# Kernel optimization log

Measured on AMD Instinct MI355X. Metric: run time of the kernel, lower is better.

The kernel has to match this reference:

```python
import jax, jax.numpy as jnp
import numpy as np
from jax import lax

B, S, D = 2, 1024, 1024
N = 16            # mamba state dim
EXPAND = 2
DI = EXPAND * D   # inner dim 2048
K = 4             # depthwise conv kernel
H = 16            # soliton heads
DH = D // H
DT_RANK = D // 16
SOL_DT = 0.1      # soliton integration step


def _ln(x, g, b):
    mu = jnp.mean(x, -1, keepdims=True)
    var = jnp.var(x, -1, keepdims=True)
    return (x - mu) / jnp.sqrt(var + 1e-5) * g + b


def setup_inputs() -> dict:
    key = jax.random.key(0)
    ks = jax.random.split(key, 12)
    def nrm(k, sh, sc=0.02):
        return jax.random.normal(k, sh, jnp.float32) * sc
    return {
        'x': nrm(ks[0], (B, S, D), 1.0),
        'ln1_g': jnp.ones(D), 'ln1_b': jnp.zeros(D),
        'W_in': nrm(ks[1], (D, 2 * DI)), 'b_in': jnp.zeros(2 * DI),
        'conv_w': nrm(ks[2], (DI, K), 0.1), 'conv_b': jnp.zeros(DI),
        'W_xp': nrm(ks[3], (DI, DT_RANK + 2 * N)),
        'W_dt': nrm(ks[4], (DT_RANK, DI), 0.1),
        'b_dt': jnp.full((DI,), -4.6),  # softplus(-4.6) ~ 0.01 init dt
        'A_log': jnp.log(jnp.broadcast_to(jnp.arange(1, N + 1, dtype=jnp.float32), (DI, N))),
        'D_skip': jnp.ones(DI),
        'W_out': nrm(ks[5], (DI, D)), 'b_out': jnp.zeros(D),
        'ln2_g': jnp.ones(D), 'ln2_b': jnp.zeros(D),
        'W_si': nrm(ks[6], (D, D)), 'b_si': jnp.zeros(D),
        'gates': nrm(ks[7], (H, 3), 0.1),   # per-head weights for [sine-Gordon, KdV, Heimburg-Jackson]
        'alpha': nrm(ks[8], (H,), 0.1),     # HJ nonlinearity coefficient
        'W_so': nrm(ks[9], (D, D)), 'b_so': jnp.zeros(D),
    }


def _forward(x, ln1_g, ln1_b, W_in, b_in, conv_w, conv_b, W_xp, W_dt, b_dt,
             A_log, D_skip, W_out, b_out, ln2_g, ln2_b, W_si, b_si,
             gates, alpha, W_so, b_so):
    b, s, d = x.shape
    # ---- Mamba mixer branch ----
    u = _ln(x, ln1_g, ln1_b)
    xz = u @ W_in + b_in                                   # [b,s,2*DI]
    xp, z = jnp.split(xz, 2, axis=-1)                      # [b,s,DI] each
    # causal depthwise conv along sequence
    xt = xp.transpose(0, 2, 1)                             # [b,DI,s]
    yc = lax.conv_general_dilated(xt, conv_w[:, None, :], (1,), [(K - 1, 0)],
                                  feature_group_count=DI,
                                  dimension_numbers=('NCW', 'OIW', 'NCW'))
    xc = jax.nn.silu(yc.transpose(0, 2, 1) + conv_b)       # [b,s,DI]
    dbc = xc @ W_xp
    dtr, Bs, Cs = jnp.split(dbc, [DT_RANK, DT_RANK + N], axis=-1)
    dt = jax.nn.softplus(dtr @ W_dt + b_dt)                # [b,s,DI]
    A = -jnp.exp(A_log)                                    # [DI,N]
    dA = jnp.exp(dt[..., None] * A)                        # [b,s,DI,N]
    dBx = (dt * xc)[..., None] * Bs[:, :, None, :]         # [b,s,DI,N]

    def step(h, inp):
        dA_t, dBx_t, C_t = inp
        h = dA_t * h + dBx_t                               # [b,DI,N]
        y = jnp.einsum('bdn,bn->bd', h, C_t)
        return h, y

    h0 = jnp.zeros((b, DI, N), x.dtype)
    xs = (dA.transpose(1, 0, 2, 3), dBx.transpose(1, 0, 2, 3), Cs.transpose(1, 0, 2))
    _, ys = lax.scan(step, h0, xs)
    y = ys.transpose(1, 0, 2)                              # [b,s,DI]
    y = (y + xc * D_skip) * jax.nn.silu(z)
    x = x + y @ W_out + b_out

    # ---- Soliton interaction branch ----
    v = _ln(x, ln2_g, ln2_b)
    uu = (v @ W_si + b_si).reshape(b, s, H, DH)
    up = jnp.pad(uu, ((0, 0), (2, 2), (0, 0), (0, 0)), mode='edge')
    ux = (up[:, 3:-1] - up[:, 1:-3]) * 0.5                 # central 1st derivative
    uxx = up[:, 3:-1] - 2.0 * uu + up[:, 1:-3]
    uxxx = (up[:, 4:] - 2.0 * up[:, 3:-1] + 2.0 * up[:, 1:-3] - up[:, :-4]) * 0.5
    sg = jnp.sin(uu)                                       # sine-Gordon
    kdv = -6.0 * uu * ux - uxxx                            # KdV
    hj = (1.0 + alpha[None, None, :, None] * uu) * uxx     # Heimburg-Jackson
    du = (gates[None, None, :, 0:1] * sg
          + gates[None, None, :, 1:2] * kdv
          + gates[None, None, :, 2:3] * hj)
    sol = (SOL_DT * du).reshape(b, s, d) @ W_so + b_so
    return x + sol


def reference(x, ln1_g, ln1_b, W_in, b_in, conv_w, conv_b, W_xp, W_dt, b_dt,
              A_log, D_skip, W_out, b_out, ln2_g, ln2_b, W_si, b_si,
              gates, alpha, W_so, b_so):
    return _forward(x, ln1_g, ln1_b, W_in, b_in, conv_w, conv_b, W_xp, W_dt, b_dt,
                    A_log, D_skip, W_out, b_out, ln2_g, ln2_b, W_si, b_si,
                    gates, alpha, W_so, b_so)
```

## Files before the change

kernel.cpp:

```cpp
#include <hip/hip_runtime.h>
#include <hip/hip_bf16.h>
#include <math.h>

typedef unsigned short u16;
typedef unsigned int u32;
typedef __attribute__((ext_vector_type(8))) short short8;
typedef __attribute__((ext_vector_type(4))) float f32x4;

constexpr int CB = 2;
constexpr int CS = 1024;
constexpr int CD = 1024;
constexpr int CDI = 2048;
constexpr int CNC2 = 64;
constexpr int CL2 = 16;

__device__ inline u16 f2bf(float v) {
  __hip_bfloat16 h = __float2bfloat16(v);
  return *reinterpret_cast<u16*>(&h);
}
__device__ inline float bf2f(u16 v) {
  return __uint_as_float(((u32)v) << 16);
}

__device__ inline void gload16(const void* g, void* l) {
  __builtin_amdgcn_global_load_lds((const __attribute__((address_space(1))) void*)g,
                                   (__attribute__((address_space(3))) void*)l, 16, 0, 0);
}

struct TJob { const float* src; u16* dst; int K, N, gx, base; };
struct TJobs { TJob j[6]; };

__global__ __launch_bounds__(256)
void transpose_all_kernel(TJobs jobs) {
  int b = blockIdx.x;
  int ji = 0;
#pragma unroll
  for (int i = 1; i < 6; ++i) if (b >= jobs.j[i].base) ji = i;
  TJob jb = jobs.j[ji];
  int lb = b - jb.base;
  int n0 = (lb % jb.gx) * 32, k0 = (lb / jb.gx) * 32;
  __shared__ float tile[32][33];
  int tx = threadIdx.x & 31, ty = threadIdx.x >> 5;
#pragma unroll
  for (int i = 0; i < 4; ++i) {
    int k = k0 + ty + i * 8, n = n0 + tx;
    tile[ty + i * 8][tx] = (n < jb.N) ? jb.src[(size_t)k * jb.N + n] : 0.f;
  }
  __syncthreads();
#pragma unroll
  for (int i = 0; i < 4; ++i) {
    int n = n0 + ty + i * 8, k = k0 + tx;
    jb.dst[(size_t)n * jb.K + k] = f2bf(tile[tx][ty + i * 8]);
  }
}

__global__ __launch_bounds__(256)
void ln_kernel(const float* __restrict__ x, const float* __restrict__ g,
               const float* __restrict__ bb, u16* __restrict__ outb) {
  int row = blockIdx.x;
  const float4* xr = (const float4*)(x + (size_t)row * CD);
  float4 v = xr[threadIdx.x];
  float s = v.x + v.y + v.z + v.w;
  float ss = v.x * v.x + v.y * v.y + v.z * v.z + v.w * v.w;
#pragma unroll
  for (int o = 1; o < 64; o <<= 1) { s += __shfl_xor(s, o); ss += __shfl_xor(ss, o); }
  __shared__ float sb[4], ssb[4];
  int wid = threadIdx.x >> 6;
  if ((threadIdx.x & 63) == 0) { sb[wid] = s; ssb[wid] = ss; }
  __syncthreads();
  s = sb[0] + sb[1] + sb[2] + sb[3];
  ss = ssb[0] + ssb[1] + ssb[2] + ssb[3];
  float mu = s * (1.f / CD);
  float var = ss * (1.f / CD) - mu * mu;
  float rstd = rsqrtf(var + 1e-5f);
  float4 gv = ((const float4*)g)[threadIdx.x];
  float4 bv = ((const float4*)bb)[threadIdx.x];
  ushort4 o;
  o.x = f2bf((v.x - mu) * rstd * gv.x + bv.x);
  o.y = f2bf((v.y - mu) * rstd * gv.y + bv.y);
  o.z = f2bf((v.z - mu) * rstd * gv.z + bv.z);
  o.w = f2bf((v.w - mu) * rstd * gv.w + bv.w);
  ((ushort4*)(outb + (size_t)row * CD))[threadIdx.x] = o;
}

__global__ __launch_bounds__(256)
void ln_fuse_kernel(const float* __restrict__ x, const float* __restrict__ S0,
                    const float* __restrict__ S1, const float* __restrict__ bo,
                    const float* __restrict__ g, const float* __restrict__ bb,
                    float* __restrict__ out, u16* __restrict__ outb) {
  int row = blockIdx.x;
  float4 xv = ((const float4*)(x + (size_t)row * CD))[threadIdx.x];
  float4 s0 = ((const float4*)(S0 + (size_t)row * CD))[threadIdx.x];
  float4 s1 = ((const float4*)(S1 + (size_t)row * CD))[threadIdx.x];
  float4 bv0 = ((const float4*)bo)[threadIdx.x];
  float4 v;
  v.x = xv.x + s0.x + s1.x + bv0.x;
  v.y = xv.y + s0.y + s1.y + bv0.y;
  v.z = xv.z + s0.z + s1.z + bv0.z;
  v.w = xv.w + s0.w + s1.w + bv0.w;
  ((float4*)(out + (size_t)row * CD))[threadIdx.x] = v;
  float s = v.x + v.y + v.z + v.w;
  float ss = v.x * v.x + v.y * v.y + v.z * v.z + v.w * v.w;
#pragma unroll
  for (int o = 1; o < 64; o <<= 1) { s += __shfl_xor(s, o); ss += __shfl_xor(ss, o); }
  __shared__ float sb[4], ssb[4];
  int wid = threadIdx.x >> 6;
  if ((threadIdx.x & 63) == 0) { sb[wid] = s; ssb[wid] = ss; }
  __syncthreads();
  s = sb[0] + sb[1] + sb[2] + sb[3];
  ss = ssb[0] + ssb[1] + ssb[2] + ssb[3];
  float mu = s * (1.f / CD);
  float var = ss * (1.f / CD) - mu * mu;
  float rstd = rsqrtf(var + 1e-5f);
  float4 gv = ((const float4*)g)[threadIdx.x];
  float4 bv = ((const float4*)bb)[threadIdx.x];
  ushort4 o;
  o.x = f2bf((v.x - mu) * rstd * gv.x + bv.x);
  o.y = f2bf((v.y - mu) * rstd * gv.y + bv.y);
  o.z = f2bf((v.z - mu) * rstd * gv.z + bv.z);
  o.w = f2bf((v.w - mu) * rstd * gv.w + bv.w);
  ((ushort4*)(outb + (size_t)row * CD))[threadIdx.x] = o;
}

__global__ __launch_bounds__(256)
void add3_kernel(float* __restrict__ out, const float* __restrict__ S0,
                 const float* __restrict__ S1, const float* __restrict__ bias) {
  int idx = blockIdx.x * 256 + threadIdx.x;
  int c4 = idx & 255;
  float4 o = ((const float4*)out)[idx];
  float4 a = ((const float4*)S0)[idx];
  float4 b = ((const float4*)S1)[idx];
  float4 bv = ((const float4*)bias)[c4];
  o.x += a.x + b.x + bv.x;
  o.y += a.y + b.y + bv.y;
  o.z += a.z + b.z + bv.z;
  o.w += a.w + b.w + bv.w;
  ((float4*)out)[idx] = o;
}

template<int BN, int LDA, int LDB>
__global__ __launch_bounds__(256)
void gemm5_kernel(const u16* __restrict__ A, const u16* __restrict__ Bt,
                  const float* __restrict__ bias,
                  const float* __restrict__ resid, int ldr,
                  float* __restrict__ C, int ldc,
                  u16* __restrict__ aux, int auxN,
                  int partial_stride, int Nact, int K, int act) {
  constexpr int WN = BN / 32;
  constexpr int AHALF = 128 * 32;
  constexpr int BHALF = BN * 32;
  __shared__ __align__(16) u16 As[2 * AHALF];
  __shared__ __align__(16) u16 Bs[2 * BHALF];
  const int tid = threadIdx.x, lane = tid & 63, wid = tid >> 6;
  const int wr = wid >> 1, wc = wid & 1;
  int nwg = gridDim.x * gridDim.y;
  int bid = blockIdx.y * gridDim.x + blockIdx.x;
  int swz = (bid & 7) * (nwg >> 3) + (bid >> 3);
  int bx = swz % gridDim.x, by = swz / gridDim.x;
  const int bm = by * 128, bn = bx * BN;
  const int kper = K / gridDim.z;
  const int kbeg = blockIdx.z * kper;
  const int nt = kper / 32;

  int a_src[2], b_src[BN / 64];
#pragma unroll
  for (int j = 0; j < 2; ++j) {
    int c = tid + j * 256;
    int row = c >> 2, kc = (c & 3) ^ ((row + (row >> 2)) & 3);
    a_src[j] = (bm + row) * LDA + kc * 8 + kbeg;
  }
#pragma unroll
  for (int j = 0; j < BN / 64; ++j) {
    int c = tid + j * 256;
    int row = c >> 2, kc = (c & 3) ^ ((row + (row >> 2)) & 3);
    b_src[j] = (bn + row) * LDB + kc * 8 + kbeg;
  }
  int afo[4], bfo[WN];
  const int ch = lane >> 4;
#pragma unroll
  for (int m = 0; m < 4; ++m) {
    int r = wr * 64 + m * 16 + (lane & 15);
    afo[m] = r * 32 + ((ch ^ ((r + (r >> 2)) & 3)) << 3);
  }
#pragma unroll
  for (int n = 0; n < WN; ++n) {
    int r = wc * (BN / 2) + n * 16 + (lane & 15);
    bfo[n] = r * 32 + ((ch ^ ((r + (r >> 2)) & 3)) << 3);
  }
  f32x4 acc[4][WN] = {};

  auto stage = [&](int t, int abuf, int bbuf) {
    int k0 = t * 32;
#pragma unroll
    for (int j = 0; j < 2; ++j)
      gload16(A + a_src[j] + k0, As + abuf + (tid + j * 256) * 8);
#pragma unroll
    for (int j = 0; j < BN / 64; ++j)
      gload16(Bt + b_src[j] + k0, Bs + bbuf + (tid + j * 256) * 8);
  };
  auto compute = [&](int abuf, int bbuf) {
    short8 af[4], bfr[WN];
#pragma unroll
    for (int m = 0; m < 4; ++m) af[m] = *(const short8*)&As[abuf + afo[m]];
#pragma unroll
    for (int n = 0; n < WN; ++n) bfr[n] = *(const short8*)&Bs[bbuf + bfo[n]];
#pragma unroll
    for (int m = 0; m < 4; ++m)
#pragma unroll
      for (int n = 0; n < WN; ++n)
        acc[m][n] = __builtin_amdgcn_mfma_f32_16x16x32_bf16(af[m], bfr[n], acc[m][n], 0, 0, 0);
  };

  stage(0, 0, 0);
  __syncthreads();
  int t = 0;
  while (true) {
    if (t + 1 < nt) stage(t + 1, AHALF, BHALF);
    compute(0, 0);
    __syncthreads();
    if (++t == nt) break;
    if (t + 1 < nt) stage(t + 1, 0, 0);
    compute(AHALF, BHALF);
    __syncthreads();
    if (++t == nt) break;
  }

  const int fr = lane & 15, fq = lane >> 4;
  const int ksegs = gridDim.z;
  float* Cz = C + (size_t)blockIdx.z * partial_stride;
#pragma unroll
  for (int m = 0; m < 4; ++m) {
#pragma unroll
    for (int n = 0; n < WN; ++n) {
#pragma unroll
      for (int j = 0; j < 4; ++j) {
        int row = bm + wr * 64 + m * 16 + fq * 4 + j;
        int col = bn + wc * (BN / 2) + n * 16 + fr;
        if (col < Nact) {
          float v = acc[m][n][j];
          if (ksegs == 1) {
            if (bias) v += bias[col];
            if (resid) v += resid[(size_t)row * ldr + col];
            if (act == 1) v = (v > 20.f) ? v : log1pf(__expf(v));
            if (C) C[(size_t)row * ldc + col] = v;
            if (aux && col < auxN) aux[(size_t)row * auxN + col] = f2bf(v);
          } else if (partial_stride > 0) {
            Cz[(size_t)row * ldc + col] = v;
          } else {
            atomicAdd(&C[(size_t)row * ldc + col], v);
          }
        }
      }
    }
  }
}

__global__ __launch_bounds__(256)
void conv_silu_kernel(const u16* __restrict__ xz, const float* __restrict__ w,
                      const float* __restrict__ cb, u16* __restrict__ xcb) {
  int idx = blockIdx.x * 256 + threadIdx.x;
  int d0 = (idx & 255) * 8;
  int t = (idx >> 8) & (CS - 1);
  int b = idx >> 18;
  const u16* base = xz + (size_t)(b * CS) * 4096 + d0;
  float acc[8];
  float4 cb2[2] = { ((const float4*)(cb + d0))[0], ((const float4*)(cb + d0))[1] };
#pragma unroll
  for (int i = 0; i < 8; ++i) acc[i] = ((const float*)cb2)[i];
#pragma unroll
  for (int k = 0; k < 4; ++k) {
    int tt = t - 3 + k;
    if (tt >= 0) {
      short8 v = *(const short8*)(base + (size_t)tt * 4096);
#pragma unroll
      for (int i = 0; i < 8; ++i)
        acc[i] = fmaf(bf2f((u16)v[i]), w[(d0 + i) * 4 + k], acc[i]);
    }
  }
  short8 o;
#pragma unroll
  for (int i = 0; i < 8; ++i) {
    float v = acc[i] * (1.f / (1.f + __expf(-acc[i])));
    o[i] = (short)f2bf(v);
  }
  *(short8*)(xcb + (size_t)(b * CS + t) * CDI + d0) = o;
}

__global__ __launch_bounds__(256)
void dtr_convert_kernel(const float* __restrict__ dbc, u16* __restrict__ dtrb) {
  int idx = blockIdx.x * 256 + threadIdx.x;
  int r = idx >> 6, k = idx & 63;
  dtrb[idx] = f2bf(dbc[r * 96 + k]);
}

__global__ __launch_bounds__(256)
void scan1_kernel(const u16* __restrict__ dtb, const u16* __restrict__ xcb,
                  const float* __restrict__ dbc, const float* __restrict__ A_log,
                  u16* __restrict__ P, u16* __restrict__ Q) {
  int gid = blockIdx.x * 256 + threadIdx.x;
  int d = gid & (CDI - 1);
  int c = (gid >> 11) & (CNC2 - 1);
  int b = gid >> 17;
  float acoef[16];
#pragma unroll
  for (int j = 0; j < 4; ++j) {
    float4 al = ((const float4*)(A_log + d * 16))[j];
    acoef[j * 4 + 0] = -__expf(al.x);
    acoef[j * 4 + 1] = -__expf(al.y);
    acoef[j * 4 + 2] = -__expf(al.z);
    acoef[j * 4 + 3] = -__expf(al.w);
  }
  float Pv[16], Qv[16];
#pragma unroll
  for (int n = 0; n < 16; ++n) { Pv[n] = 1.f; Qv[n] = 0.f; }
  size_t rowbase = (size_t)b * CS + (size_t)c * CL2;
  for (int i = 0; i < CL2; ++i) {
    size_t r = rowbase + i;
    float dtv = bf2f(dtb[r * CDI + d]);
    float xcv = bf2f(xcb[r * CDI + d]);
    float dx = dtv * xcv;
    const float4* bs4 = (const float4*)(dbc + r * 96 + 64);
    float bs[16];
#pragma unroll
    for (int j = 0; j < 4; ++j) {
      float4 t4 = bs4[j];
      bs[j * 4 + 0] = t4.x; bs[j * 4 + 1] = t4.y; bs[j * 4 + 2] = t4.z; bs[j * 4 + 3] = t4.w;
    }
#pragma unroll
    for (int n = 0; n < 16; ++n) {
      float a = __expf(dtv * acoef[n]);
      Pv[n] *= a;
      Qv[n] = fmaf(a, Qv[n], dx * bs[n]);
    }
  }
  size_t o = (((size_t)b * CNC2 + c) * CDI + d) * 16;
  u16 pb[16], qb[16];
#pragma unroll
  for (int n = 0; n < 16; ++n) { pb[n] = f2bf(Pv[n]); qb[n] = f2bf(Qv[n]); }
#pragma unroll
  for (int j = 0; j < 2; ++j) {
    *(short8*)(P + o + j * 8) = *(short8*)(pb + j * 8);
    *(short8*)(Q + o + j * 8) = *(short8*)(qb + j * 8);
  }
}

__global__ __launch_bounds__(256)
void scan2_kernel(const u16* __restrict__ P, u16* __restrict__ Q) {
  int gid = blockIdx.x * 256 + threadIdx.x;
  int n = gid & 15;
  int d = (gid >> 4) & (CDI - 1);
  int b = gid >> 15;
  int obase = ((b * CNC2) * CDI + d) * 16 + n;
  constexpr int CSTRIDE = CDI * 16;
  float h = 0.f;
  for (int c0 = 0; c0 < CNC2; c0 += 8) {
    float pv[8], qv[8];
#pragma unroll
    for (int i = 0; i < 8; ++i) {
      int o = obase + (c0 + i) * CSTRIDE;
      pv[i] = bf2f(P[o]);
      qv[i] = bf2f(Q[o]);
    }
#pragma unroll
    for (int i = 0; i < 8; ++i) {
      int o = obase + (c0 + i) * CSTRIDE;
      Q[o] = f2bf(h);
      h = fmaf(pv[i], h, qv[i]);
    }
  }
}

__global__ __launch_bounds__(256)
void scan3_kernel(const u16* __restrict__ dtb, const u16* __restrict__ xcb,
                  const float* __restrict__ dbc, const float* __restrict__ A_log,
                  const u16* __restrict__ Q, const u16* __restrict__ xz,
                  const float* __restrict__ Dskip, u16* __restrict__ y2b) {
  int gid = blockIdx.x * 256 + threadIdx.x;
  int d = gid & (CDI - 1);
  int c = (gid >> 11) & (CNC2 - 1);
  int b = gid >> 17;
  float acoef[16];
#pragma unroll
  for (int j = 0; j < 4; ++j) {
    float4 al = ((const float4*)(A_log + d * 16))[j];
    acoef[j * 4 + 0] = -__expf(al.x);
    acoef[j * 4 + 1] = -__expf(al.y);
    acoef[j * 4 + 2] = -__expf(al.z);
    acoef[j * 4 + 3] = -__expf(al.w);
  }
  float h[16];
  size_t o = (((size_t)b * CNC2 + c) * CDI + d) * 16;
#pragma unroll
  for (int j = 0; j < 2; ++j) {
    short8 q8 = *(const short8*)(Q + o + j * 8);
#pragma unroll
    for (int n = 0; n < 8; ++n) h[j * 8 + n] = bf2f((u16)q8[n]);
  }
  float dsk = Dskip[d];
  size_t rowbase = (size_t)b * CS + (size_t)c * CL2;
  for (int i = 0; i < CL2; ++i) {
    size_t r = rowbase + i;
    float dtv = bf2f(dtb[r * CDI + d]);
    float xcv = bf2f(xcb[r * CDI + d]);
    float zv = bf2f(xz[r * 4096 + 2048 + d]);
    float dx = dtv * xcv;
    const float4* bc4 = (const float4*)(dbc + r * 96 + 64);
    float bs[16], cs[16];
#pragma unroll
    for (int j = 0; j < 4; ++j) {
      float4 t4 = bc4[j];
      bs[j * 4 + 0] = t4.x; bs[j * 4 + 1] = t4.y; bs[j * 4 + 2] = t4.z; bs[j * 4 + 3] = t4.w;
      float4 u4 = bc4[4 + j];
      cs[j * 4 + 0] = u4.x; cs[j * 4 + 1] = u4.y; cs[j * 4 + 2] = u4.z; cs[j * 4 + 3] = u4.w;
    }
    float y = 0.f;
#pragma unroll
    for (int n = 0; n < 16; ++n) {
      float a = __expf(dtv * acoef[n]);
      h[n] = fmaf(a, h[n], dx * bs[n]);
      y = fmaf(h[n], cs[n], y);
    }
    float sz = zv * (1.f / (1.f + __expf(-zv)));
    y2b[r * CDI + d] = f2bf((y + xcv * dsk) * sz);
  }
}

__global__ __launch_bounds__(256)
void soliton_kernel(const float* __restrict__ Sa, const float* __restrict__ Sb,
                    const float* __restrict__ bsi, const float* __restrict__ gates,
                    const float* __restrict__ alpha, u16* __restrict__ sol) {
  int idx = blockIdx.x * 256 + threadIdx.x;
  int d = idx & (CD - 1);
  int t = (idx >> 10) & (CS - 1);
  int b = idx >> 20;
  int h = d >> 6;
  size_t base = (size_t)b * CS * CD + d;
  int tm2 = max(t - 2, 0), tm1 = max(t - 1, 0);
  int tp1 = min(t + 1, CS - 1), tp2 = min(t + 2, CS - 1);
  float um2 = Sa[base + (size_t)tm2 * CD] + Sb[base + (size_t)tm2 * CD];
  float um1 = Sa[base + (size_t)tm1 * CD] + Sb[base + (size_t)tm1 * CD];
  float u0r = Sa[base + (size_t)t   * CD] + Sb[base + (size_t)t   * CD];
  float up1 = Sa[base + (size_t)tp1 * CD] + Sb[base + (size_t)tp1 * CD];
  float up2 = Sa[base + (size_t)tp2 * CD] + Sb[base + (size_t)tp2 * CD];
  float u0 = u0r + bsi[d];
  float ux   = (up1 - um1) * 0.5f;
  float uxx  = up1 - 2.f * u0r + um1;
  float uxxx = (up2 - 2.f * up1 + 2.f * um1 - um2) * 0.5f;
  float sg = sinf(u0);
  float kdv = -6.f * u0 * ux - uxxx;
  float hj = (1.f + alpha[h] * u0) * uxx;
  float du = gates[h * 3 + 0] * sg + gates[h * 3 + 1] * kdv + gates[h * 3 + 2] * hj;
  sol[idx] = f2bf(0.1f * du);
}

extern "C" void kernel_launch(void* const* d_in, const int* in_sizes, int n_in,
                              void* d_out, int out_size, void* d_ws, size_t ws_size,
                              hipStream_t stream) {
  const float* x      = (const float*)d_in[0];
  const float* ln1_g  = (const float*)d_in[1];
  const float* ln1_b  = (const float*)d_in[2];
  const float* W_in   = (const float*)d_in[3];
  const float* b_in   = (const float*)d_in[4];
  const float* conv_w = (const float*)d_in[5];
  const float* conv_b = (const float*)d_in[6];
  const float* W_xp   = (const float*)d_in[7];
  const float* W_dt   = (const float*)d_in[8];
  const float* b_dt   = (const float*)d_in[9];
  const float* A_log  = (const float*)d_in[10];
  const float* D_skip = (const float*)d_in[11];
  const float* W_out  = (const float*)d_in[12];
  const float* b_out  = (const float*)d_in[13];
  const float* ln2_g  = (const float*)d_in[14];
  const float* ln2_b  = (const float*)d_in[15];
  const float* W_si   = (const float*)d_in[16];
  const float* b_si   = (const float*)d_in[17];
  const float* gates  = (const float*)d_in[18];
  const float* alpha  = (const float*)d_in[19];
  const float* W_so   = (const float*)d_in[20];
  const float* b_so   = (const float*)d_in[21];
  float* out = (float*)d_out;

  float* ws = (float*)d_ws;
  size_t off = 0;
  auto alloc = [&](size_t nwords) { float* p = ws + off; off += nwords; return p; };
  const size_t BS = (size_t)CB * CS;
  const size_t M1 = 1024 * 1024;

  u16* Wt_in  = (u16*)alloc(2 * M1);
  u16* Wt_xp  = (u16*)alloc(128 * 1024);
  u16* Wt_dt  = (u16*)alloc(64 * 1024);
  u16* Wt_out = (u16*)alloc(M1);
  u16* Wt_si  = (u16*)alloc(M1 / 2);
  u16* Wt_so  = (u16*)alloc(M1 / 2);
  u16* u_bf   = (u16*)alloc(M1);
  u16* sol_bf = u_bf;
  u16* xz_bf  = (u16*)alloc(4 * M1);
  u16* dt_bf  = (u16*)alloc(2 * M1);
  u16* xc_bf  = (u16*)alloc(2 * M1);
  float* dbc  = alloc(BS * 96);
  u16* dtr_bf = (u16*)alloc(64 * 1024);
  float* Pb_f = alloc(2 * M1);
  float* Qb_f = alloc(2 * M1);
  u16* Pb = (u16*)Pb_f;
  u16* Qb = (u16*)Qb_f;
  u16* y2_bf  = (u16*)alloc(2 * M1);

  dim3 blk(256);
  const int PSTRIDE = (int)(BS * CD);

  {
    TJobs jobs;
    int base = 0;
    auto mk = [&](const float* s, u16* dst, int K, int N) {
      int gx = (N + 31) / 32, gy = K / 32;
      TJob j{s, dst, K, N, gx, base};
      base += gx * gy;
      return j;
    };
    jobs.j[0] = mk(W_in, Wt_in, 1024, 4096);
    jobs.j[1] = mk(W_xp, Wt_xp, 2048, 96);
    jobs.j[2] = mk(W_dt, Wt_dt, 64, 2048);
    jobs.j[3] = mk(W_out, Wt_out, 2048, 1024);
    jobs.j[4] = mk(W_si, Wt_si, 1024, 1024);
    jobs.j[5] = mk(W_so, Wt_so, 1024, 1024);
    hipMemsetAsync(Wt_xp, 0, 128 * 2048 * sizeof(u16), stream);
    transpose_all_kernel<<<base, blk, 0, stream>>>(jobs);
  }

  ln_kernel<<<BS, blk, 0, stream>>>(x, ln1_g, ln1_b, u_bf);
  gemm5_kernel<64, 1024, 1024><<<dim3(64, 16), blk, 0, stream>>>(
      u_bf, Wt_in, b_in, nullptr, 0, nullptr, 0, xz_bf, 4096, 0, 4096, 1024, 0);
  conv_silu_kernel<<<(BS * CDI) / (256 * 8), blk, 0, stream>>>(xz_bf, conv_w, conv_b, xc_bf);
  hipMemsetAsync(dbc, 0, BS * 96 * sizeof(float), stream);
  gemm5_kernel<128, 2048, 2048><<<dim3(1, 16, 16), blk, 0, stream>>>(
      xc_bf, Wt_xp, nullptr, nullptr, 0, dbc, 96, nullptr, 0, 0, 96, 2048, 0);
  dtr_convert_kernel<<<(BS * 64) / 256, blk, 0, stream>>>(dbc, dtr_bf);
  gemm5_kernel<64, 64, 64><<<dim3(32, 16), blk, 0, stream>>>(
      dtr_bf, Wt_dt, b_dt, nullptr, 0, nullptr, 0, dt_bf, 2048, 0, 2048, 64, 1);
  scan1_kernel<<<(CB * CNC2 * CDI) / 256, blk, 0, stream>>>(dt_bf, xc_bf, dbc, A_log, Pb, Qb);
  scan2_kernel<<<(CB * CDI * 16) / 256, blk, 0, stream>>>(Pb, Qb);
  scan3_kernel<<<(CB * CNC2 * CDI) / 256, blk, 0, stream>>>(dt_bf, xc_bf, dbc, A_log, Qb, xz_bf, D_skip, y2_bf);
  gemm5_kernel<64, 2048, 2048><<<dim3(16, 16, 2), blk, 0, stream>>>(
      y2_bf, Wt_out, nullptr, nullptr, 0, Pb_f, CD, nullptr, 0, PSTRIDE, 1024, 2048, 0);
  ln_fuse_kernel<<<BS, blk, 0, stream>>>(x, Pb_f, Qb_f, b_out, ln2_g, ln2_b, out, u_bf);
  gemm5_kernel<64, 1024, 1024><<<dim3(16, 16, 2), blk, 0, stream>>>(
      u_bf, Wt_si, nullptr, nullptr, 0, Pb_f, CD, nullptr, 0, PSTRIDE, 1024, 1024, 0);
  soliton_kernel<<<(BS * CD) / 256, blk, 0, stream>>>(Pb_f, Qb_f, b_si, gates, alpha, sol_bf);
  gemm5_kernel<64, 1024, 1024><<<dim3(16, 16, 2), blk, 0, stream>>>(
      sol_bf, Wt_so, nullptr, nullptr, 0, Pb_f, CD, nullptr, 0, PSTRIDE, 1024, 1024, 0);
  add3_kernel<<<(BS * CD) / (256 * 4), blk, 0, stream>>>(out, Pb_f, Qb_f, b_so);
}
```

Measured before the change: 271.9 us.

## Use BK=64 GEMM tiles with XOR swizzle and split-K partials for x_proj

The GEMM kernel now stages 64-wide K slices per iteration instead of 32, with an 8-way XOR swizzle in LDS. This halves the number of barriers and pipeline steps per tile. The x_proj GEMM no longer zeroes an output and accumulates into it with atomics; it writes 16 split-K partial buffers, and a new combine kernel sums them and also produces the bf16 dt_rank input. This drops a memset and the atomic contention, at the cost of extra memory traffic for the partials. The transpose now writes the padding rows of the x_proj weight itself instead of relying on a separate memset.

```diff
diff --git a/kernel.cpp b/kernel.cpp
--- a/kernel.cpp
+++ b/kernel.cpp
@@ -138,17 +138,16 @@
   ((float4*)out)[idx] = o;
 }
 
-template<int BN, int LDA, int LDB>
-__global__ __launch_bounds__(256)
-void gemm5_kernel(const u16* __restrict__ A, const u16* __restrict__ Bt,
+template<int LDA, int LDB>
+__global__ __launch_bounds__(256)
+void gemm6_kernel(const u16* __restrict__ A, const u16* __restrict__ Bt,
                   const float* __restrict__ bias,
                   const float* __restrict__ resid, int ldr,
                   float* __restrict__ C, int ldc,
                   u16* __restrict__ aux, int auxN,
                   int partial_stride, int Nact, int K, int act) {
-  constexpr int WN = BN / 32;
-  constexpr int AHALF = 128 * 32;
-  constexpr int BHALF = BN * 32;
+  constexpr int AHALF = 128 * 64;
+  constexpr int BHALF = 64 * 64;
   __shared__ __align__(16) u16 As[2 * AHALF];
   __shared__ __align__(16) u16 Bs[2 * BHALF];
   const int tid = threadIdx.x, lane = tid & 63, wid = tid >> 6;
@@ -157,58 +156,61 @@
   int bid = blockIdx.y * gridDim.x + blockIdx.x;
   int swz = (bid & 7) * (nwg >> 3) + (bid >> 3);
   int bx = swz % gridDim.x, by = swz / gridDim.x;
-  const int bm = by * 128, bn = bx * BN;
+  const int bm = by * 128, bn = bx * 64;
   const int kper = K / gridDim.z;
   const int kbeg = blockIdx.z * kper;
-  const int nt = kper / 32;
-
-  int a_src[2], b_src[BN / 64];
+  const int nt = kper / 64;
+
+  int a_src[4], b_src[2];
+#pragma unroll
+  for (int j = 0; j < 4; ++j) {
+    int c = tid + j * 256;
+    int row = c >> 3, kc = (c & 7) ^ (row & 7);
+    a_src[j] = (bm + row) * LDA + kc * 8 + kbeg;
+  }
 #pragma unroll
   for (int j = 0; j < 2; ++j) {
     int c = tid + j * 256;
-    int row = c >> 2, kc = (c & 3) ^ ((row + (row >> 2)) & 3);
-    a_src[j] = (bm + row) * LDA + kc * 8 + kbeg;
-  }
-#pragma unroll
-  for (int j = 0; j < BN / 64; ++j) {
-    int c = tid + j * 256;
-    int row = c >> 2, kc = (c & 3) ^ ((row + (row >> 2)) & 3);
+    int row = c >> 3, kc = (c & 7) ^ (row & 7);
     b_src[j] = (bn + row) * LDB + kc * 8 + kbeg;
   }
-  int afo[4], bfo[WN];
+  int afo[4], bfo[2];
   const int ch = lane >> 4;
 #pragma unroll
   for (int m = 0; m < 4; ++m) {
     int r = wr * 64 + m * 16 + (lane & 15);
-    afo[m] = r * 32 + ((ch ^ ((r + (r >> 2)) & 3)) << 3);
-  }
-#pragma unroll
-  for (int n = 0; n < WN; ++n) {
-    int r = wc * (BN / 2) + n * 16 + (lane & 15);
-    bfo[n] = r * 32 + ((ch ^ ((r + (r >> 2)) & 3)) << 3);
-  }
-  f32x4 acc[4][WN] = {};
+    afo[m] = r * 64 + ((ch ^ (r & 7)) << 3);
+  }
+#pragma unroll
+  for (int n = 0; n < 2; ++n) {
+    int r = wc * 32 + n * 16 + (lane & 15);
+    bfo[n] = r * 64 + ((ch ^ (r & 7)) << 3);
+  }
+  f32x4 acc[4][2] = {};
 
   auto stage = [&](int t, int abuf, int bbuf) {
-    int k0 = t * 32;
+    int k0 = t * 64;
+#pragma unroll
+    for (int j = 0; j < 4; ++j)
+      gload16(A + a_src[j] + k0, As + abuf + (tid + j * 256) * 8);
 #pragma unroll
     for (int j = 0; j < 2; ++j)
-      gload16(A + a_src[j] + k0, As + abuf + (tid + j * 256) * 8);
-#pragma unroll
-    for (int j = 0; j < BN / 64; ++j)
       gload16(Bt + b_src[j] + k0, Bs + bbuf + (tid + j * 256) * 8);
   };
   auto compute = [&](int abuf, int bbuf) {
-    short8 af[4], bfr[WN];
-#pragma unroll
-    for (int m = 0; m < 4; ++m) af[m] = *(const short8*)&As[abuf + afo[m]];
-#pragma unroll
-    for (int n = 0; n < WN; ++n) bfr[n] = *(const short8*)&Bs[bbuf + bfo[n]];
-#pragma unroll
-    for (int m = 0; m < 4; ++m)
-#pragma unroll
-      for (int n = 0; n < WN; ++n)
-        acc[m][n] = __builtin_amdgcn_mfma_f32_16x16x32_bf16(af[m], bfr[n], acc[m][n], 0, 0, 0);
+#pragma unroll
+    for (int ks = 0; ks < 2; ++ks) {
+      short8 af[4], bfr[2];
+#pragma unroll
+      for (int m = 0; m < 4; ++m) af[m] = *(const short8*)&As[abuf + (afo[m] ^ (ks * 32))];
+#pragma unroll
+      for (int n = 0; n < 2; ++n) bfr[n] = *(const short8*)&Bs[bbuf + (bfo[n] ^ (ks * 32))];
+#pragma unroll
+      for (int m = 0; m < 4; ++m)
+#pragma unroll
+        for (int n = 0; n < 2; ++n)
+          acc[m][n] = __builtin_amdgcn_mfma_f32_16x16x32_bf16(af[m], bfr[n], acc[m][n], 0, 0, 0);
+    }
   };
 
   stage(0, 0, 0);
@@ -231,11 +233,11 @@
 #pragma unroll
   for (int m = 0; m < 4; ++m) {
 #pragma unroll
-    for (int n = 0; n < WN; ++n) {
+    for (int n = 0; n < 2; ++n) {
 #pragma unroll
       for (int j = 0; j < 4; ++j) {
         int row = bm + wr * 64 + m * 16 + fq * 4 + j;
-        int col = bn + wc * (BN / 2) + n * 16 + fr;
+        int col = bn + wc * 32 + n * 16 + fr;
         if (col < Nact) {
           float v = acc[m][n][j];
           if (ksegs == 1) {
@@ -287,10 +289,23 @@
 }
 
 __global__ __launch_bounds__(256)
-void dtr_convert_kernel(const float* __restrict__ dbc, u16* __restrict__ dtrb) {
+void dbc_combine_kernel(const float* __restrict__ parts, float* __restrict__ dbc,
+                        u16* __restrict__ dtrb) {
   int idx = blockIdx.x * 256 + threadIdx.x;
-  int r = idx >> 6, k = idx & 63;
-  dtrb[idx] = f2bf(dbc[r * 96 + k]);
+  int row = idx / 24, c4 = idx % 24;
+  int o = row * 96 + c4 * 4;
+  float4 s = make_float4(0.f, 0.f, 0.f, 0.f);
+#pragma unroll
+  for (int z = 0; z < 16; ++z) {
+    float4 v = *(const float4*)(parts + (size_t)z * (2048 * 96) + o);
+    s.x += v.x; s.y += v.y; s.z += v.z; s.w += v.w;
+  }
+  *(float4*)(dbc + o) = s;
+  if (c4 < 16) {
+    ushort4 b;
+    b.x = f2bf(s.x); b.y = f2bf(s.y); b.z = f2bf(s.z); b.w = f2bf(s.w);
+    *(ushort4*)(dtrb + row * 64 + c4 * 4) = b;
+  }
 }
 
 __global__ __launch_bounds__(256)
@@ -507,46 +522,45 @@
 
   dim3 blk(256);
   const int PSTRIDE = (int)(BS * CD);
+  const int DBC_STRIDE = 2048 * 96;
 
   {
     TJobs jobs;
     int base = 0;
-    auto mk = [&](const float* s, u16* dst, int K, int N) {
-      int gx = (N + 31) / 32, gy = K / 32;
+    auto mk = [&](const float* s, u16* dst, int K, int N, int Npad) {
+      int gx = Npad / 32, gy = K / 32;
       TJob j{s, dst, K, N, gx, base};
       base += gx * gy;
       return j;
     };
-    jobs.j[0] = mk(W_in, Wt_in, 1024, 4096);
-    jobs.j[1] = mk(W_xp, Wt_xp, 2048, 96);
-    jobs.j[2] = mk(W_dt, Wt_dt, 64, 2048);
-    jobs.j[3] = mk(W_out, Wt_out, 2048, 1024);
-    jobs.j[4] = mk(W_si, Wt_si, 1024, 1024);
-    jobs.j[5] = mk(W_so, Wt_so, 1024, 1024);
-    hipMemsetAsync(Wt_xp, 0, 128 * 2048 * sizeof(u16), stream);
+    jobs.j[0] = mk(W_in, Wt_in, 1024, 4096, 4096);
+    jobs.j[1] = mk(W_xp, Wt_xp, 2048, 96, 128);
+    jobs.j[2] = mk(W_dt, Wt_dt, 64, 2048, 2048);
+    jobs.j[3] = mk(W_out, Wt_out, 2048, 1024, 1024);
+    jobs.j[4] = mk(W_si, Wt_si, 1024, 1024, 1024);
+    jobs.j[5] = mk(W_so, Wt_so, 1024, 1024, 1024);
     transpose_all_kernel<<<base, blk, 0, stream>>>(jobs);
   }
 
   ln_kernel<<<BS, blk, 0, stream>>>(x, ln1_g, ln1_b, u_bf);
-  gemm5_kernel<64, 1024, 1024><<<dim3(64, 16), blk, 0, stream>>>(
+  gemm6_kernel<1024, 1024><<<dim3(64, 16), blk, 0, stream>>>(
       u_bf, Wt_in, b_in, nullptr, 0, nullptr, 0, xz_bf, 4096, 0, 4096, 1024, 0);
   conv_silu_kernel<<<(BS * CDI) / (256 * 8), blk, 0, stream>>>(xz_bf, conv_w, conv_b, xc_bf);
-  hipMemsetAsync(dbc, 0, BS * 96 * sizeof(float), stream);
-  gemm5_kernel<128, 2048, 2048><<<dim3(1, 16, 16), blk, 0, stream>>>(
-      xc_bf, Wt_xp, nullptr, nullptr, 0, dbc, 96, nullptr, 0, 0, 96, 2048, 0);
-  dtr_convert_kernel<<<(BS * 64) / 256, blk, 0, stream>>>(dbc, dtr_bf);
-  gemm5_kernel<64, 64, 64><<<dim3(32, 16), blk, 0, stream>>>(
+  gemm6_kernel<2048, 2048><<<dim3(2, 16, 16), blk, 0, stream>>>(
+      xc_bf, Wt_xp, nullptr, nullptr, 0, Pb_f, 96, nullptr, 0, DBC_STRIDE, 96, 2048, 0);
+  dbc_combine_kernel<<<(2048 * 24) / 256, blk, 0, stream>>>(Pb_f, dbc, dtr_bf);
+  gemm6_kernel<64, 64><<<dim3(32, 16), blk, 0, stream>>>(
       dtr_bf, Wt_dt, b_dt, nullptr, 0, nullptr, 0, dt_bf, 2048, 0, 2048, 64, 1);
   scan1_kernel<<<(CB * CNC2 * CDI) / 256, blk, 0, stream>>>(dt_bf, xc_bf, dbc, A_log, Pb, Qb);
   scan2_kernel<<<(CB * CDI * 16) / 256, blk, 0, stream>>>(Pb, Qb);
   scan3_kernel<<<(CB * CNC2 * CDI) / 256, blk, 0, stream>>>(dt_bf, xc_bf, dbc, A_log, Qb, xz_bf, D_skip, y2_bf);
-  gemm5_kernel<64, 2048, 2048><<<dim3(16, 16, 2), blk, 0, stream>>>(
+  gemm6_kernel<2048, 2048><<<dim3(16, 16, 2), blk, 0, stream>>>(
       y2_bf, Wt_out, nullptr, nullptr, 0, Pb_f, CD, nullptr, 0, PSTRIDE, 1024, 2048, 0);
   ln_fuse_kernel<<<BS, blk, 0, stream>>>(x, Pb_f, Qb_f, b_out, ln2_g, ln2_b, out, u_bf);
-  gemm5_kernel<64, 1024, 1024><<<dim3(16, 16, 2), blk, 0, stream>>>(
+  gemm6_kernel<1024, 1024><<<dim3(16, 16, 2), blk, 0, stream>>>(
       u_bf, Wt_si, nullptr, nullptr, 0, Pb_f, CD, nullptr, 0, PSTRIDE, 1024, 1024, 0);
   soliton_kernel<<<(BS * CD) / 256, blk, 0, stream>>>(Pb_f, Qb_f, b_si, gates, alpha, sol_bf);
-  gemm5_kernel<64, 1024, 1024><<<dim3(16, 16, 2), blk, 0, stream>>>(
+  gemm6_kernel<1024, 1024><<<dim3(16, 16, 2), blk, 0, stream>>>(
       sol_bf, Wt_so, nullptr, nullptr, 0, Pb_f, CD, nullptr, 0, PSTRIDE, 1024, 1024, 0);
   add3_kernel<<<(BS * CD) / (256 * 4), blk, 0, stream>>>(out, Pb_f, Qb_f, b_so);
 }
```

Result: faster. 254.3 us (-6.5%).
